# Performance work log

Hardware: AMD Instinct MI355X
Metric: run time of the kernel (lower is better)

The kernel has to match this reference:

```python
import jax, jax.numpy as jnp
import numpy as np
import math

B, T, D, H = 4, 2048, 1024, 16
HD = D // H  # 64
EPS = 1e-5


def layernorm(x, g, b):
    mu = jnp.mean(x, axis=-1, keepdims=True)
    var = jnp.var(x, axis=-1, keepdims=True)
    return (x - mu) * jax.lax.rsqrt(var + EPS) * g + b


def setup_inputs() -> dict:
    key = jax.random.key(0)
    ks = jax.random.split(key, 6)
    s = 0.02
    return {
        "inputs": jax.random.normal(ks[0], (B, T, D), jnp.float32),
        "Wq": jax.random.normal(ks[1], (H, D, HD), jnp.float32) * s,
        "Wk": jax.random.normal(ks[2], (H, D, HD), jnp.float32) * s,
        "Wv": jax.random.normal(ks[3], (H, D, HD), jnp.float32) * s,
        "W1": jax.random.normal(ks[4], (D, 4 * D), jnp.float32) * s,
        "b1": jnp.zeros((4 * D,), jnp.float32),
        "W2": jax.random.normal(ks[5], (4 * D, D), jnp.float32) * s,
        "b2": jnp.zeros((D,), jnp.float32),
        "g1": jnp.ones((D,), jnp.float32),
        "be1": jnp.zeros((D,), jnp.float32),
        "g2": jnp.ones((D,), jnp.float32),
        "be2": jnp.zeros((D,), jnp.float32),
    }


def reference(inputs, Wq, Wk, Wv, W1, b1, W2, b2, g1, be1, g2, be2):
    Tq = inputs.shape[1]
    norm_inputs = layernorm(inputs, g1, be1)
    # per-head projections, vectorized over heads: [B, H, T, HD]
    q = jnp.einsum('btd,hde->bhte', norm_inputs, Wq)
    k = jnp.einsum('btd,hde->bhte', norm_inputs, Wk)
    v = jnp.einsum('btd,hde->bhte', norm_inputs, Wv)
    scores = jnp.einsum('bhte,bhse->bhts', q, k) / math.sqrt(HD)
    causal = jnp.tril(jnp.ones((Tq, Tq), bool))
    scores = jnp.where(causal, scores, -jnp.inf)
    attn = jax.nn.softmax(scores, axis=-1)  # dropout = identity (eval mode)
    o = jnp.einsum('bhts,bhse->bhte', attn, v)
    # concat heads along feature dim (head-major, matches torch.concat over head outputs)
    attn_out = o.transpose(0, 2, 1, 3).reshape(inputs.shape[0], Tq, D)
    x = inputs + attn_out
    norm_x = layernorm(x, g2, be2)
    ff = jax.nn.relu(norm_x @ W1 + b1) @ W2 + b2
    return x + ff
```

## Files before the change

### kernel.cpp

```cpp
#include <hip/hip_runtime.h>
#include <hip/hip_bf16.h>


#define B_  4
#define T_  2048
#define D_  1024
#define H_  16

typedef float  f32x4  __attribute__((ext_vector_type(4)));
typedef __bf16 bf16x8 __attribute__((ext_vector_type(8)));
typedef short  s16x8  __attribute__((ext_vector_type(8)));
typedef short  s16x4  __attribute__((ext_vector_type(4)));

#define MFMA(a,b,c) __builtin_amdgcn_mfma_f32_16x16x32_bf16((a),(b),(c),0,0,0)

__device__ __forceinline__ short f2bf(float f) {
  __bf16 h = (__bf16)f;
  return __builtin_bit_cast(short, h);
}
__device__ __forceinline__ float bf2f(short s) {
  return (float)__builtin_bit_cast(__bf16, s);
}

__device__ __forceinline__ void gload16(const void* g, void* l) {
  __builtin_amdgcn_global_load_lds(
      (__attribute__((address_space(1))) void*)g,
      (__attribute__((address_space(3))) void*)l, 16, 0, 0);
}

__global__ __launch_bounds__(256) void ln_kernel(
    const float* __restrict__ in, const short* __restrict__ res,
    const float* __restrict__ gamma, const float* __restrict__ beta,
    short* __restrict__ xout, short* __restrict__ nout)
{
  const int row = blockIdx.x, t = threadIdx.x;
  const size_t base = (size_t)row * 1024;
  float4 v = *(const float4*)&in[base + t*4];
  if (res) {
    const s16x4 r2 = *(const s16x4*)&res[base + t*4];
    v.x += bf2f(r2[0]); v.y += bf2f(r2[1]); v.z += bf2f(r2[2]); v.w += bf2f(r2[3]);
  }
  if (xout) {
    s16x4 xo;
    xo[0] = f2bf(v.x); xo[1] = f2bf(v.y); xo[2] = f2bf(v.z); xo[3] = f2bf(v.w);
    *(s16x4*)&xout[base + t*4] = xo;
  }
  float s  = v.x + v.y + v.z + v.w;
  float ss = v.x*v.x + v.y*v.y + v.z*v.z + v.w*v.w;
  #pragma unroll
  for (int off = 32; off > 0; off >>= 1) { s += __shfl_down(s, off); ss += __shfl_down(ss, off); }
  __shared__ float red[8];
  const int w = t >> 6, l = t & 63;
  if (l == 0) { red[w] = s; red[w + 4] = ss; }
  __syncthreads();
  s  = red[0] + red[1] + red[2] + red[3];
  ss = red[4] + red[5] + red[6] + red[7];
  const float mu   = s * (1.0f/1024.0f);
  const float rstd = rsqrtf(ss * (1.0f/1024.0f) - mu*mu + 1e-5f);
  const float4 gm = *(const float4*)&gamma[t*4];
  const float4 bt = *(const float4*)&beta[t*4];
  s16x4 o;
  o[0] = f2bf((v.x - mu) * rstd * gm.x + bt.x);
  o[1] = f2bf((v.y - mu) * rstd * gm.y + bt.y);
  o[2] = f2bf((v.z - mu) * rstd * gm.z + bt.z);
  o[3] = f2bf((v.w - mu) * rstd * gm.w + bt.w);
  *(s16x4*)&nout[base + t*4] = o;
}

__global__ __launch_bounds__(256) void prep_wqkv(
    const float* __restrict__ Wq, const float* __restrict__ Wk,
    const float* __restrict__ Wv, short* __restrict__ outT)
{
  const int p = blockIdx.z, h = blockIdx.y, d0 = blockIdx.x * 32;
  const float* W = (p == 0 ? Wq : (p == 1 ? Wk : Wv)) + (size_t)h * 1024 * 64;
  __shared__ float tile[32][65];
  const int t = threadIdx.x;
  #pragma unroll
  for (int i = 0; i < 8; ++i) {
    const int idx = t + i*256, d = idx >> 6, e = idx & 63;
    tile[d][e] = W[(size_t)(d0 + d) * 64 + e];
  }
  __syncthreads();
  #pragma unroll
  for (int i = 0; i < 8; ++i) {
    const int idx = t + i*256, e = idx >> 5, d = idx & 31;
    outT[(size_t)(p*1024 + h*64 + e) * 1024 + d0 + d] = f2bf(tile[d][e]);
  }
}

__global__ __launch_bounds__(256) void transpose_conv(
    const float* __restrict__ in, short* __restrict__ out, int R, int C)
{
  __shared__ float tile[64][65];
  const int c0 = blockIdx.x * 64, r0 = blockIdx.y * 64;
  const int t = threadIdx.x;
  #pragma unroll
  for (int i = 0; i < 16; ++i) {
    const int idx = t + i*256, r = idx >> 6, c = idx & 63;
    tile[r][c] = in[(size_t)(r0 + r) * C + c0 + c];
  }
  __syncthreads();
  #pragma unroll
  for (int i = 0; i < 16; ++i) {
    const int idx = t + i*256, c = idx >> 6, r = idx & 63;
    out[(size_t)(c0 + c) * R + r0 + r] = f2bf(tile[r][c]);
  }
}

template<int EPI, int NT>
__global__ __launch_bounds__(512) void gemm256(
    const short* __restrict__ A, const short* __restrict__ BT,
    const float* __restrict__ bias, const short* __restrict__ resid,
    void* __restrict__ Cout, short* __restrict__ vt, int M, int N, int K, int nx)
{
  __shared__ short ldsA[3][256*64];
  __shared__ short ldsB[3][128*64];
  const int tid = threadIdx.x;
  const int w = tid >> 6, l = tid & 63, g = l >> 4, ln = l & 15;
  const int wm = w >> 2, wn = w & 3;

  const int nwg = gridDim.x;
  const int sw = (blockIdx.x & 7) * (nwg >> 3) + (blockIdx.x >> 3);
  const int m0 = (sw / nx) * 256, n0 = (sw % nx) * 128;

  const short* srcA[4];
  const short* srcB[2];
  #pragma unroll
  for (int i = 0; i < 4; ++i) {
    const int c = i*512 + tid, row = c >> 3;
    srcA[i] = A + (size_t)(m0 + row) * K + ((c & 7) ^ (row & 7)) * 8;
  }
  #pragma unroll
  for (int i = 0; i < 2; ++i) {
    const int c = i*512 + tid, row = c >> 3;
    srcB[i] = BT + (size_t)(n0 + row) * K + ((c & 7) ^ (row & 7)) * 8;
  }
  const int ofsA = w * 64 * 8;
  #define STAGE_A(i_, t_) gload16(srcA[i_] + (t_)*64, &ldsA[(t_) % 3][(i_)*4096 + ofsA])
  #define STAGE_B(i_, t_) gload16(srcB[i_] + (t_)*64, &ldsB[(t_) % 3][(i_)*4096 + ofsA])
  #define STAGE_P0(t_) do { STAGE_A(0,t_); STAGE_A(1,t_); STAGE_B(0,t_); } while (0)
  #define STAGE_P1(t_) do { STAGE_A(2,t_); STAGE_A(3,t_); STAGE_B(1,t_); } while (0)

  STAGE_P0(0); STAGE_P1(0);
  STAGE_P0(1); STAGE_P1(1);

  f32x4 zero = {0.f,0.f,0.f,0.f};
  f32x4 acc[8][2];
  #pragma unroll
  for (int i = 0; i < 8; ++i) { acc[i][0] = zero; acc[i][1] = zero; }

  for (int t = 0; t < NT; ++t) {
    if (t < NT-1) asm volatile("s_waitcnt vmcnt(6)" ::: "memory");
    else          asm volatile("s_waitcnt vmcnt(0)" ::: "memory");
    __builtin_amdgcn_s_barrier();
    __builtin_amdgcn_sched_barrier(0);
    const short* Ab = &ldsA[t % 3][0];
    const short* Bb = &ldsB[t % 3][0];

    #pragma unroll
    for (int kk = 0; kk < 2; ++kk) {
      const int rsl = ((kk*4 + g) ^ (ln & 7)) * 8;
      bf16x8 bfr[2], af[8];
      #pragma unroll
      for (int nt = 0; nt < 2; ++nt)
        bfr[nt] = *(const bf16x8*)&Bb[(wn*32 + nt*16 + ln)*64 + rsl];
      #pragma unroll
      for (int mi = 0; mi < 8; ++mi)
        af[mi] = *(const bf16x8*)&Ab[(wm*128 + mi*16 + ln)*64 + rsl];
      if (t + 2 < NT) { if (kk == 0) STAGE_P0(t+2); else STAGE_P1(t+2); }
      __builtin_amdgcn_sched_barrier(0);
      __builtin_amdgcn_s_setprio(1);
      #pragma unroll
      for (int mi = 0; mi < 8; ++mi)
        #pragma unroll
        for (int nt = 0; nt < 2; ++nt)
          acc[mi][nt] = MFMA(af[mi], bfr[nt], acc[mi][nt]);
      __builtin_amdgcn_s_setprio(0);
      __builtin_amdgcn_sched_barrier(0);
    }
  }
  #undef STAGE_P1
  #undef STAGE_P0
  #undef STAGE_B
  #undef STAGE_A

  #pragma unroll
  for (int mi = 0; mi < 8; ++mi) {
    #pragma unroll
    for (int nt = 0; nt < 2; ++nt) {
      #pragma unroll
      for (int r = 0; r < 4; ++r) {
        const size_t rr = (size_t)(m0 + wm*128 + mi*16 + g*4 + r);
        const int    cc = n0 + wn*32 + nt*16 + ln;
        float v = acc[mi][nt][r];
        if constexpr (EPI == 0) {
          if (cc >= 2048) {
            const int f = cc - 2048, hh = f >> 6, e = f & 63;
            const int bb = (int)(rr >> 11), tt = (int)(rr & 2047);
            vt[(((size_t)bb*16 + hh)*64 + e)*2048 + tt] = f2bf(v);
          } else {
            if (cc < 1024) v *= 0.18033688f;
            ((short*)Cout)[rr * N + cc] = f2bf(v);
          }
        } else if constexpr (EPI == 1) {
          v += bias[cc]; v = fmaxf(v, 0.f);
          ((short*)Cout)[rr * N + cc] = f2bf(v);
        } else {
          v += bias[cc] + bf2f(resid[rr * N + cc]);
          ((float*)Cout)[rr * N + cc] = v;
        }
      }
    }
  }
}

__global__ __launch_bounds__(256) void attn_kernel(
    const short* __restrict__ qkv, const short* __restrict__ vt,
    short* __restrict__ out)
{
  __shared__ short Ks[2][64*64];
  __shared__ short Vs[64*64];
  __shared__ short Ps[4][32*64];
  const int id = blockIdx.x;
  const int jq = id >> 8, r256 = id & 255;
  const int q8 = r256 & 7, b32 = r256 >> 3;
  const int qt = (jq == 0) ? q8 : (jq == 1) ? 8 + q8 : (jq == 2) ? 15 - q8 : 7 - q8;
  const int bh = (jq < 2) ? b32 : 32 + b32;
  const int b = bh >> 4, h = bh & 15;
  const int tid = threadIdx.x;
  const int w = tid >> 6, l = tid & 63, g = l >> 4, ln = l & 15;
  const int qr0 = qt*128 + w*32;
  const size_t rowb = (size_t)b * T_;
  const short* vtb = vt + (((size_t)b*16 + h)*64) * 2048;

  bf16x8 qf[2][2];
  #pragma unroll
  for (int mi = 0; mi < 2; ++mi) {
    const short* qp = qkv + (rowb + qr0 + mi*16 + ln) * 3072 + h*64 + g*8;
    qf[mi][0] = *(const bf16x8*)qp;
    qf[mi][1] = *(const bf16x8*)(qp + 32);
  }

  f32x4 zero = {0.f, 0.f, 0.f, 0.f};
  f32x4 acc_o[2][4];
  float mrow[2][4], lrow[2][4];
  #pragma unroll
  for (int mi = 0; mi < 2; ++mi)
    #pragma unroll
    for (int i = 0; i < 4; ++i) { acc_o[mi][i] = zero; mrow[mi][i] = -1e30f; lrow[mi][i] = 0.f; }

  const int nkv = 2*qt + 2;

  #define STAGE_K(kvi) do {                                                  \
    const int kv0_ = (kvi)*64;                                               \
    short* dstb_ = Ks[(kvi) & 1];                                            \
    _Pragma("unroll")                                                        \
    for (int i_ = 0; i_ < 2; ++i_) {                                         \
      const int c_ = i_*256 + w*64 + l;                                      \
      const int row_ = c_ >> 3;                                              \
      const int col8_ = ((c_ & 7) ^ (row_ & 7)) * 8;                         \
      gload16(qkv + (rowb + kv0_ + row_)*3072 + 1024 + h*64 + col8_,         \
              &dstb_[(i_*256 + w*64) * 8]);                                  \
    }                                                                        \
  } while (0)
  #define STAGE_V(kvi) do {                                                  \
    const int kv0_ = (kvi)*64;                                               \
    _Pragma("unroll")                                                        \
    for (int i_ = 0; i_ < 2; ++i_) {                                         \
      const int c_ = i_*256 + w*64 + l;                                      \
      const int row_ = c_ >> 3;                                              \
      const int col8_ = ((c_ & 7) ^ (row_ & 7)) * 8;                         \
      gload16(vtb + (size_t)row_*2048 + kv0_ + col8_,                        \
              &Vs[(i_*256 + w*64) * 8]);                                     \
    }                                                                        \
  } while (0)

  STAGE_K(0);
  STAGE_V(0);

  for (int kv = 0; kv < nkv; ++kv) {
    const int kv0 = kv * 64;
    if (kv + 1 < nkv) {
      STAGE_K(kv + 1);
      asm volatile("s_waitcnt vmcnt(2)" ::: "memory");
    } else {
      asm volatile("s_waitcnt vmcnt(0)" ::: "memory");
    }
    __builtin_amdgcn_s_barrier();
    __builtin_amdgcn_sched_barrier(0);

    if (kv0 <= qr0 + 31) {
      const short* KsB = Ks[kv & 1];
      f32x4 s[2][4];
      #pragma unroll
      for (int nt = 0; nt < 4; ++nt) {
        const int krow = nt*16 + ln;
        bf16x8 kf0 = *(const bf16x8*)&KsB[krow*64 + ((0*4 + g) ^ (ln & 7))*8];
        bf16x8 kf1 = *(const bf16x8*)&KsB[krow*64 + ((1*4 + g) ^ (ln & 7))*8];
        #pragma unroll
        for (int mi = 0; mi < 2; ++mi) {
          f32x4 a = zero;
          a = MFMA(qf[mi][0], kf0, a);
          a = MFMA(qf[mi][1], kf1, a);
          s[mi][nt] = a;
        }
      }
      if (kv0 + 63 > qr0) {
        #pragma unroll
        for (int nt = 0; nt < 4; ++nt) {
          const int kt = kv0 + nt*16 + ln;
          #pragma unroll
          for (int mi = 0; mi < 2; ++mi)
            #pragma unroll
            for (int r = 0; r < 4; ++r)
              if (kt > qr0 + mi*16 + g*4 + r) s[mi][nt][r] = -1e30f;
        }
      }
      #pragma unroll
      for (int mi = 0; mi < 2; ++mi) {
        #pragma unroll
        for (int r = 0; r < 4; ++r) {
          float mx = fmaxf(fmaxf(s[mi][0][r], s[mi][1][r]), fmaxf(s[mi][2][r], s[mi][3][r]));
          #pragma unroll
          for (int off = 1; off < 16; off <<= 1) mx = fmaxf(mx, __shfl_xor(mx, off));
          const float mnew = fmaxf(mrow[mi][r], mx);
          const float sc = __builtin_amdgcn_exp2f(mrow[mi][r] - mnew);
          mrow[mi][r] = mnew;
          float rs = 0.f;
          #pragma unroll
          for (int nt = 0; nt < 4; ++nt) {
            const float pv = __builtin_amdgcn_exp2f(s[mi][nt][r] - mnew);
            s[mi][nt][r] = pv;
            rs += pv;
          }
          #pragma unroll
          for (int off = 1; off < 16; off <<= 1) rs += __shfl_xor(rs, off);
          lrow[mi][r] = lrow[mi][r] * sc + rs;
          #pragma unroll
          for (int nt = 0; nt < 4; ++nt) acc_o[mi][nt][r] *= sc;
        }
      }
      #pragma unroll
      for (int mi = 0; mi < 2; ++mi)
        #pragma unroll
        for (int nt = 0; nt < 4; ++nt)
          #pragma unroll
          for (int r = 0; r < 4; ++r) {
            const int row = mi*16 + g*4 + r;
            const int col = nt*16 + ln;
            Ps[w][row*64 + (((col >> 3) ^ (row & 7)) << 3) + (col & 7)] = f2bf(s[mi][nt][r]);
          }
      #pragma unroll
      for (int kk = 0; kk < 2; ++kk) {
        bf16x8 pa[2];
        #pragma unroll
        for (int mi = 0; mi < 2; ++mi)
          pa[mi] = *(const bf16x8*)&Ps[w][(mi*16 + ln)*64 + (((kk*4 + g) ^ (ln & 7)) << 3)];
        #pragma unroll
        for (int nt = 0; nt < 4; ++nt) {
          const bf16x8 bv = *(const bf16x8*)&Vs[(nt*16 + ln)*64 + (((kk*4 + g) ^ (ln & 7)) << 3)];
          #pragma unroll
          for (int mi = 0; mi < 2; ++mi)
            acc_o[mi][nt] = MFMA(pa[mi], bv, acc_o[mi][nt]);
        }
      }
    }

    __builtin_amdgcn_s_barrier();
    __builtin_amdgcn_sched_barrier(0);
    if (kv + 1 < nkv) STAGE_V(kv + 1);
  }
  #undef STAGE_K
  #undef STAGE_V

  #pragma unroll
  for (int mi = 0; mi < 2; ++mi)
    #pragma unroll
    for (int r = 0; r < 4; ++r) {
      const float il = 1.0f / lrow[mi][r];
      const size_t row = rowb + qr0 + mi*16 + g*4 + r;
      #pragma unroll
      for (int nt = 0; nt < 4; ++nt)
        out[row * D_ + h*64 + nt*16 + ln] = f2bf(acc_o[mi][nt][r] * il);
    }
}

extern "C" void kernel_launch(void* const* d_in, const int* in_sizes, int n_in,
                              void* d_out, int out_size, void* d_ws, size_t ws_size,
                              hipStream_t stream)
{
  (void)in_sizes; (void)n_in; (void)out_size; (void)ws_size;
  const float* inputs = (const float*)d_in[0];
  const float* Wq  = (const float*)d_in[1];
  const float* Wk  = (const float*)d_in[2];
  const float* Wv  = (const float*)d_in[3];
  const float* W1  = (const float*)d_in[4];
  const float* b1  = (const float*)d_in[5];
  const float* W2  = (const float*)d_in[6];
  const float* b2  = (const float*)d_in[7];
  const float* g1  = (const float*)d_in[8];
  const float* be1 = (const float*)d_in[9];
  const float* g2  = (const float*)d_in[10];
  const float* be2 = (const float*)d_in[11];

  char* p = (char*)d_ws;
  short* normB = (short*)p;  p += (size_t)8192*1024*2;
  short* qkvT  = (short*)p;  p += (size_t)3072*1024*2;
  short* w1T   = (short*)p;  p += (size_t)4096*1024*2;
  short* w2T   = (short*)p;  p += (size_t)4096*1024*2;
  char*  reg   = p;          p += (size_t)8192*3072*2 + (size_t)8192*1024*2;
  short* xbuf  = (short*)p;
  short* qkv   = (short*)reg;
  short* attn  = (short*)(reg + (size_t)8192*3072*2);
  short* h1    = (short*)reg;
  short* vT    = xbuf;

  ln_kernel<<<8192, 256, 0, stream>>>(inputs, nullptr, g1, be1, nullptr, normB);
  prep_wqkv<<<dim3(32,16,3), 256, 0, stream>>>(Wq, Wk, Wv, qkvT);
  transpose_conv<<<dim3(64,16), 256, 0, stream>>>(W1, w1T, 1024, 4096);
  transpose_conv<<<dim3(16,64), 256, 0, stream>>>(W2, w2T, 4096, 1024);
  gemm256<0,16><<<768, 512, 0, stream>>>(normB, qkvT, nullptr, nullptr, qkv, vT, 8192, 3072, 1024, 24);
  attn_kernel<<<1024, 256, 0, stream>>>(qkv, vT, attn);
  ln_kernel<<<8192, 256, 0, stream>>>(inputs, attn, g2, be2, xbuf, normB);
  gemm256<1,16><<<1024, 512, 0, stream>>>(normB, w1T, b1, nullptr, h1, nullptr, 8192, 4096, 1024, 32);
  gemm256<2,64><<<256, 512, 0, stream>>>(h1, w2T, b2, xbuf, (float*)d_out, nullptr, 8192, 1024, 4096, 8);
}
```

Measured before the change: 388.0 us.

## Replace 256x128 GEMM tiles with 128x128 tiles and 32-deep K steps

The GEMM kernel is rewritten to use 128x128 output tiles with 256 threads and a K step of 32, in place of 256x128 tiles with 512 threads and a K step of 64. LDS swizzling and the wave-to-tile mapping are redone to fit, and each wave now computes a 64x64 block. The aim is more workgroups, which may help occupancy and load balance. In exchange it reloads more data from global memory per output and doubles the number of barrier-synchronised K iterations.

Result: slower. 414.4 us, median of 2 (+6.8%).

```diff
diff --git a/kernel.cpp b/kernel.cpp
--- a/kernel.cpp
+++ b/kernel.cpp
@@ -108,90 +108,87 @@
 }
 
 template<int EPI, int NT>
-__global__ __launch_bounds__(512) void gemm256(
+__global__ __launch_bounds__(256) void gemm128(
     const short* __restrict__ A, const short* __restrict__ BT,
     const float* __restrict__ bias, const short* __restrict__ resid,
     void* __restrict__ Cout, short* __restrict__ vt, int M, int N, int K, int nx)
 {
-  __shared__ short ldsA[3][256*64];
-  __shared__ short ldsB[3][128*64];
+  __shared__ short ldsA[3][128*32];
+  __shared__ short ldsB[3][128*32];
   const int tid = threadIdx.x;
   const int w = tid >> 6, l = tid & 63, g = l >> 4, ln = l & 15;
-  const int wm = w >> 2, wn = w & 3;
+  const int wm = w >> 1, wn = w & 1;
 
   const int nwg = gridDim.x;
   const int sw = (blockIdx.x & 7) * (nwg >> 3) + (blockIdx.x >> 3);
-  const int m0 = (sw / nx) * 256, n0 = (sw % nx) * 128;
-
-  const short* srcA[4];
+  const int m0 = (sw / nx) * 128, n0 = (sw % nx) * 128;
+
+  const short* srcA[2];
   const short* srcB[2];
   #pragma unroll
-  for (int i = 0; i < 4; ++i) {
-    const int c = i*512 + tid, row = c >> 3;
-    srcA[i] = A + (size_t)(m0 + row) * K + ((c & 7) ^ (row & 7)) * 8;
-  }
-  #pragma unroll
   for (int i = 0; i < 2; ++i) {
-    const int c = i*512 + tid, row = c >> 3;
-    srcB[i] = BT + (size_t)(n0 + row) * K + ((c & 7) ^ (row & 7)) * 8;
-  }
-  const int ofsA = w * 64 * 8;
-  #define STAGE_A(i_, t_) gload16(srcA[i_] + (t_)*64, &ldsA[(t_) % 3][(i_)*4096 + ofsA])
-  #define STAGE_B(i_, t_) gload16(srcB[i_] + (t_)*64, &ldsB[(t_) % 3][(i_)*4096 + ofsA])
-  #define STAGE_P0(t_) do { STAGE_A(0,t_); STAGE_A(1,t_); STAGE_B(0,t_); } while (0)
-  #define STAGE_P1(t_) do { STAGE_A(2,t_); STAGE_A(3,t_); STAGE_B(1,t_); } while (0)
-
-  STAGE_P0(0); STAGE_P1(0);
-  STAGE_P0(1); STAGE_P1(1);
+    const int c = i*256 + tid, row = c >> 2;
+    const int scol = ((c & 3) ^ ((row >> 1) & 3)) * 8;
+    srcA[i] = A  + (size_t)(m0 + row) * K + scol;
+    srcB[i] = BT + (size_t)(n0 + row) * K + scol;
+  }
+  const int ofs = w * 64 * 8;
+  #define STAGE_A(i_, t_) gload16(srcA[i_] + (t_)*32, &ldsA[(t_) % 3][(i_)*2048 + ofs])
+  #define STAGE_B(i_, t_) gload16(srcB[i_] + (t_)*32, &ldsB[(t_) % 3][(i_)*2048 + ofs])
+  #define STAGE_ALL(t_) do { STAGE_A(0,t_); STAGE_A(1,t_); STAGE_B(0,t_); STAGE_B(1,t_); } while (0)
+
+  STAGE_ALL(0);
+  STAGE_ALL(1);
 
   f32x4 zero = {0.f,0.f,0.f,0.f};
-  f32x4 acc[8][2];
-  #pragma unroll
-  for (int i = 0; i < 8; ++i) { acc[i][0] = zero; acc[i][1] = zero; }
+  f32x4 acc[4][4];
+  #pragma unroll
+  for (int i = 0; i < 4; ++i)
+    #pragma unroll
+    for (int j = 0; j < 4; ++j) acc[i][j] = zero;
 
   for (int t = 0; t < NT; ++t) {
-    if (t < NT-1) asm volatile("s_waitcnt vmcnt(6)" ::: "memory");
+    if (t < NT-1) asm volatile("s_waitcnt vmcnt(4)" ::: "memory");
     else          asm volatile("s_waitcnt vmcnt(0)" ::: "memory");
     __builtin_amdgcn_s_barrier();
     __builtin_amdgcn_sched_barrier(0);
     const short* Ab = &ldsA[t % 3][0];
     const short* Bb = &ldsB[t % 3][0];
 
-    #pragma unroll
-    for (int kk = 0; kk < 2; ++kk) {
-      const int rsl = ((kk*4 + g) ^ (ln & 7)) * 8;
-      bf16x8 bfr[2], af[8];
-      #pragma unroll
-      for (int nt = 0; nt < 2; ++nt)
-        bfr[nt] = *(const bf16x8*)&Bb[(wn*32 + nt*16 + ln)*64 + rsl];
-      #pragma unroll
-      for (int mi = 0; mi < 8; ++mi)
-        af[mi] = *(const bf16x8*)&Ab[(wm*128 + mi*16 + ln)*64 + rsl];
-      if (t + 2 < NT) { if (kk == 0) STAGE_P0(t+2); else STAGE_P1(t+2); }
-      __builtin_amdgcn_sched_barrier(0);
-      __builtin_amdgcn_s_setprio(1);
-      #pragma unroll
-      for (int mi = 0; mi < 8; ++mi)
-        #pragma unroll
-        for (int nt = 0; nt < 2; ++nt)
-          acc[mi][nt] = MFMA(af[mi], bfr[nt], acc[mi][nt]);
-      __builtin_amdgcn_s_setprio(0);
-      __builtin_amdgcn_sched_barrier(0);
-    }
-  }
-  #undef STAGE_P1
-  #undef STAGE_P0
+    bf16x8 af[4], bfr[4];
+    #pragma unroll
+    for (int mi = 0; mi < 4; ++mi) {
+      const int row = wm*64 + mi*16 + ln;
+      af[mi] = *(const bf16x8*)&Ab[row*32 + ((g ^ ((row >> 1) & 3)))*8];
+    }
+    #pragma unroll
+    for (int nt = 0; nt < 4; ++nt) {
+      const int row = wn*64 + nt*16 + ln;
+      bfr[nt] = *(const bf16x8*)&Bb[row*32 + ((g ^ ((row >> 1) & 3)))*8];
+    }
+    if (t + 2 < NT) STAGE_ALL(t+2);
+    __builtin_amdgcn_sched_barrier(0);
+    __builtin_amdgcn_s_setprio(1);
+    #pragma unroll
+    for (int mi = 0; mi < 4; ++mi)
+      #pragma unroll
+      for (int nt = 0; nt < 4; ++nt)
+        acc[mi][nt] = MFMA(af[mi], bfr[nt], acc[mi][nt]);
+    __builtin_amdgcn_s_setprio(0);
+    __builtin_amdgcn_sched_barrier(0);
+  }
+  #undef STAGE_ALL
   #undef STAGE_B
   #undef STAGE_A
 
   #pragma unroll
-  for (int mi = 0; mi < 8; ++mi) {
-    #pragma unroll
-    for (int nt = 0; nt < 2; ++nt) {
+  for (int mi = 0; mi < 4; ++mi) {
+    #pragma unroll
+    for (int nt = 0; nt < 4; ++nt) {
       #pragma unroll
       for (int r = 0; r < 4; ++r) {
-        const size_t rr = (size_t)(m0 + wm*128 + mi*16 + g*4 + r);
-        const int    cc = n0 + wn*32 + nt*16 + ln;
+        const size_t rr = (size_t)(m0 + wm*64 + mi*16 + g*4 + r);
+        const int    cc = n0 + wn*64 + nt*16 + ln;
         float v = acc[mi][nt][r];
         if constexpr (EPI == 0) {
           if (cc >= 2048) {
@@ -419,9 +416,9 @@
   prep_wqkv<<<dim3(32,16,3), 256, 0, stream>>>(Wq, Wk, Wv, qkvT);
   transpose_conv<<<dim3(64,16), 256, 0, stream>>>(W1, w1T, 1024, 4096);
   transpose_conv<<<dim3(16,64), 256, 0, stream>>>(W2, w2T, 4096, 1024);
-  gemm256<0,16><<<768, 512, 0, stream>>>(normB, qkvT, nullptr, nullptr, qkv, vT, 8192, 3072, 1024, 24);
+  gemm128<0,32><<<1536, 256, 0, stream>>>(normB, qkvT, nullptr, nullptr, qkv, vT, 8192, 3072, 1024, 24);
   attn_kernel<<<1024, 256, 0, stream>>>(qkv, vT, attn);
   ln_kernel<<<8192, 256, 0, stream>>>(inputs, attn, g2, be2, xbuf, normB);
-  gemm256<1,16><<<1024, 512, 0, stream>>>(normB, w1T, b1, nullptr, h1, nullptr, 8192, 4096, 1024, 32);
-  gemm256<2,64><<<256, 512, 0, stream>>>(h1, w2T, b2, xbuf, (float*)d_out, nullptr, 8192, 1024, 4096, 8);
-}
+  gemm128<1,32><<<2048, 256, 0, stream>>>(normB, w1T, b1, nullptr, h1, nullptr, 8192, 4096, 1024, 32);
+  gemm128<2,128><<<512, 256, 0, stream>>>(h1, w2T, b2, xbuf, (float*)d_out, nullptr, 8192, 1024, 4096, 8);
+}
```
